# Kernel tuning notes

Measured on AMD Instinct MI355X. Metric: run time of the kernel, lower is better.

The kernel has to match this reference:

```python
import jax, jax.numpy as jnp
import numpy as np
import math

B, N, CS, CZ = 1, 512, 384, 128
GD = 16            # ipa_conf.c_hidden -> num 3D groups G
CH = GD * 3        # per-head hidden = 48
H = 8
PQ, PV = 8, 12
NF = 4             # num_frequencies
INF, EPS = 1e5, 1e-8
CZ4 = CZ // 4


def base_frequencies(num_freqs=NF, base=8.0, max_freq=1.0):
    fs = [min(base ** (-2 * i / num_freqs) * max_freq, max_freq) for i in range(num_freqs)]
    return jnp.asarray(fs, dtype=jnp.float32)


def hat(v):
    # v: [..., 3] -> skew-symmetric [..., 3, 3]
    x, y, z = v[..., 0], v[..., 1], v[..., 2]
    o = jnp.zeros_like(x)
    return jnp.stack([
        jnp.stack([o, -z, y], -1),
        jnp.stack([z, o, -x], -1),
        jnp.stack([-y, x, o], -1)], -2)


def setup_inputs() -> dict:
    key = jax.random.key(0)
    ks = jax.random.split(key, 24)
    std = 0.02
    hc = CH * H
    hpkv = H * (PQ + PV) * 3
    inp = {
        's': jax.random.normal(ks[0], (B, N, CS), jnp.float32),
        'z': jax.random.normal(ks[1], (B, N, N, CZ), jnp.float32),
        'rotvec': jax.random.normal(ks[2], (B, N, 3), jnp.float32),
        'mask': jnp.ones((B, N), jnp.float32),
        'wq': jax.random.normal(ks[3], (CS, hc), jnp.float32) * std,
        'bq': jnp.zeros((hc,), jnp.float32),
        'wkv': jax.random.normal(ks[4], (CS, 2 * hc), jnp.float32) * std,
        'bkv': jnp.zeros((2 * hc,), jnp.float32),
        'wkvp': jax.random.normal(ks[5], (CS, hpkv), jnp.float32) * std,
        'bkvp': jnp.zeros((hpkv,), jnp.float32),
        'wb': jax.random.normal(ks[6], (CZ, H), jnp.float32) * std,
        'bb': jnp.zeros((H,), jnp.float32),
        'wdz': jax.random.normal(ks[7], (CZ, CZ4), jnp.float32) * std,
        'bdz': jnp.zeros((CZ4,), jnp.float32),
        'wout': jax.random.normal(ks[8], (H * (CZ4 + CH + PV * 4), CS), jnp.float32) * std,
        'bout': jnp.zeros((CS,), jnp.float32),
        'log_freq_adj': jax.random.normal(ks[9], (NF,), jnp.float32) * std,
        'group_weights': jax.random.normal(ks[10], (GD,), jnp.float32) * std,
        'freq_weights': jnp.full((NF,), 1.0 / NF, jnp.float32),
    }
    return inp


def reference(s, z, rotvec, mask, wq, bq, wkv, bkv, wkvp, bkvp, wb, bb,
              wdz, bdz, wout, bout, log_freq_adj, group_weights, freq_weights):
    G = GD
    # projections
    q = (s @ wq + bq).reshape(B, N, H, CH)
    kv = (s @ wkv + bkv).reshape(B, N, H, 2 * CH)
    k, v = kv[..., :CH], kv[..., CH:]
    P = PQ + PV
    kvp = (s @ wkvp + bkvp).reshape(B, N, 3, H * P)      # torch split(...,3)+stack(-1)
    kvp = jnp.moveaxis(kvp, -2, -1).reshape(B, N, H, P, 3)
    v_pts = kvp[..., PQ:, :]                             # [B,N,H,PV,3]
    bias = z @ wb + bb                                   # [B,N,N,H]
    # RoPE-inspired multi-frequency Rodrigues rotations
    nrm = jnp.linalg.norm(rotvec, axis=-1, keepdims=True)
    angle = nrm + 1e-8                                   # [B,N,1]
    axis = rotvec / jnp.maximum(nrm, 1e-12)
    freqs = base_frequencies() * jnp.exp(log_freq_adj)   # [F]
    theta = angle * freqs                                # [B,N,F]
    K = hat(axis)                                        # [B,N,3,3]
    K2 = K @ K
    sin_t = jnp.sin(theta)[..., None, None]              # [B,N,F,1,1]
    cos_t = jnp.cos(theta)[..., None, None]
    I3 = jnp.eye(3, dtype=s.dtype)
    R = I3 + sin_t * K[:, :, None] + (1.0 - cos_t) * K2[:, :, None]  # [B,N,F,3,3]
    qg = q.reshape(B, N, H, G, 3)
    kg = k.reshape(B, N, H, G, 3)
    q_rot = jnp.einsum('bnfij,bnhgj->bnhgfi', R, qg)     # [B,N,H,G,F,3]
    k_rot = jnp.einsum('bnfij,bnhgj->bnhgfi', R, kg)
    # aggregation weights (sum over groups, softmax-weighted freqs)
    freq_w = jax.nn.softmax(freq_weights)
    group_w = jax.nn.softplus(group_weights) * math.sqrt(1.0 / G)
    qw = q_rot * freq_w[None, None, None, None, :, None] * group_w[None, None, None, :, None, None]
    scores = jnp.einsum('bihgfc,bjhgfc->bhij', qw, k_rot) / math.sqrt(3.0)
    a = scores + math.sqrt(1.0 / 3.0) * jnp.transpose(bias, (0, 3, 1, 2))
    sq_mask = INF * (mask[:, :, None] * mask[:, None, :] - 1.0)
    a = jax.nn.softmax(a + sq_mask[:, None], axis=-1)    # [B,H,N,N]
    # outputs
    o = jnp.einsum('bhij,bjhc->bihc', a, v).reshape(B, N, H * CH)
    o_pt = jnp.einsum('bhij,bjhpc->bihpc', a, v_pts)     # [B,N,H,PV,3]
    o_pt_norm = jnp.sqrt(jnp.sum(o_pt ** 2, -1) + EPS).reshape(B, N, H * PV)
    o_pt_flat = o_pt.reshape(B, N, H * PV, 3)
    pair_z = z @ wdz + bdz                               # [B,N,N,CZ4]
    o_pair = jnp.einsum('bhij,bijc->bihc', a, pair_z).reshape(B, N, H * CZ4)
    feats = jnp.concatenate([o, o_pt_flat[..., 0], o_pt_flat[..., 1],
                             o_pt_flat[..., 2], o_pt_norm, o_pair], axis=-1)
    return feats @ wout + bout                           # [B,N,CS]
```

## Files before the change

kernel.cpp:

```cpp
#include <hip/hip_runtime.h>
#include <math.h>


#define OFF_PROJ 0
#define SZ_PROJ (512*1632)
#define OFF_QW (OFF_PROJ + SZ_PROJ)
#define SZ_QW (8*512*192)
#define OFF_KST (OFF_QW + SZ_QW)
#define OFF_V (OFF_KST + SZ_QW)
#define SZ_V (512*384)
#define OFF_VP (OFF_V + SZ_V)
#define SZ_VP (512*288)
#define OFF_A (OFF_VP + SZ_VP)
#define SZ_A (8*512*512)
#define OFF_FEATS (OFF_A + SZ_A)
#define SZ_FEATS (512*1024)
#define OFF_PART (OFF_FEATS + SZ_FEATS)
#define SZ_PART (8*512*384)

__global__ __launch_bounds__(256) void proj_kernel(
    const float* __restrict__ s, const float* __restrict__ wq, const float* __restrict__ bq,
    const float* __restrict__ wkv, const float* __restrict__ bkv,
    const float* __restrict__ wkvp, const float* __restrict__ bkvp,
    float* __restrict__ proj)
{
  __shared__ float sT[384][34];
  int ct = blockIdx.x;
  int i0 = blockIdx.y * 32;
  int col0 = ct * 64;
  const float* W; const float* bias; int wld, wcol0;
  if (col0 < 384)       { W = wq;   bias = bq;   wld = 384; wcol0 = col0; }
  else if (col0 < 1152) { W = wkv;  bias = bkv;  wld = 768; wcol0 = col0 - 384; }
  else                  { W = wkvp; bias = bkvp; wld = 480; wcol0 = col0 - 1152; }
  int t = threadIdx.x;
  #pragma unroll
  for (int r = 0; r < 12; r++){
    int e = t + 256*r;
    int i = e & 31;
    int k4 = e >> 5;
    float4 v = *(const float4*)(s + (size_t)(i0 + i)*384 + k4*4);
    sT[k4*4+0][i] = v.x; sT[k4*4+1][i] = v.y; sT[k4*4+2][i] = v.z; sT[k4*4+3][i] = v.w;
  }
  __syncthreads();
  int cr = t & 15;
  int ipair = t >> 4;
  int ii = ipair * 2;
  int wc = wcol0 + cr*4;
  bool valid = (wc + 4 <= wld);
  int wcc = valid ? wc : (wld - 4);
  float acc[2][4];
  #pragma unroll
  for (int q = 0; q < 2; q++)
    #pragma unroll
    for (int p = 0; p < 4; p++) acc[q][p] = 0.f;
  #pragma unroll 4
  for (int k = 0; k < 384; k++){
    float2 a2 = *(const float2*)&sT[k][ii];
    float4 w4 = *(const float4*)(W + (size_t)k*wld + wcc);
    acc[0][0] = fmaf(a2.x, w4.x, acc[0][0]);
    acc[0][1] = fmaf(a2.x, w4.y, acc[0][1]);
    acc[0][2] = fmaf(a2.x, w4.z, acc[0][2]);
    acc[0][3] = fmaf(a2.x, w4.w, acc[0][3]);
    acc[1][0] = fmaf(a2.y, w4.x, acc[1][0]);
    acc[1][1] = fmaf(a2.y, w4.y, acc[1][1]);
    acc[1][2] = fmaf(a2.y, w4.z, acc[1][2]);
    acc[1][3] = fmaf(a2.y, w4.w, acc[1][3]);
  }
  if (valid){
    float4 bv = *(const float4*)(bias + wc);
    #pragma unroll
    for (int q = 0; q < 2; q++){
      int row = i0 + ii + q;
      float4 o;
      o.x = acc[q][0] + bv.x; o.y = acc[q][1] + bv.y;
      o.z = acc[q][2] + bv.z; o.w = acc[q][3] + bv.w;
      *(float4*)(proj + (size_t)row*1632 + col0 + cr*4) = o;
    }
  }
}

__global__ __launch_bounds__(128) void node_kernel(
    const float* __restrict__ proj, const float* __restrict__ rotvec,
    const float* __restrict__ lfa, const float* __restrict__ gwts, const float* __restrict__ fwts,
    float* __restrict__ Qw, float* __restrict__ Kst, float* __restrict__ V, float* __restrict__ VP)
{
  int i = blockIdx.x, t = threadIdx.x;
  const float* pr = proj + (size_t)i*1632;
  float rx = rotvec[i*3], ry = rotvec[i*3+1], rz = rotvec[i*3+2];
  float nrm = sqrtf(rx*rx + ry*ry + rz*rz);
  float angle = nrm + 1e-8f;
  float inv = 1.0f / fmaxf(nrm, 1e-12f);
  float ax = rx*inv, ay = ry*inv, az = rz*inv;
  float f0 = fwts[0], f1 = fwts[1], f2 = fwts[2], f3 = fwts[3];
  float mfw = fmaxf(fmaxf(f0,f1), fmaxf(f2,f3));
  float e0 = expf(f0-mfw), e1 = expf(f1-mfw), e2 = expf(f2-mfw), e3 = expf(f3-mfw);
  float esum = e0+e1+e2+e3;
  float fw[4] = {e0/esum, e1/esum, e2/esum, e3/esum};
  float fq[4] = { 1.0f*expf(lfa[0]), 0.35355339059327373f*expf(lfa[1]),
                  0.125f*expf(lfa[2]), 0.04419417382415922f*expf(lfa[3]) };
  int h = t >> 4, g = t & 15;
  float gw = log1pf(expf(gwts[g])) * 0.25f;
  float q0 = pr[h*48 + g*3 + 0], q1 = pr[h*48 + g*3 + 1], q2 = pr[h*48 + g*3 + 2];
  float k0 = pr[384 + h*96 + g*3 + 0], k1 = pr[384 + h*96 + g*3 + 1], k2 = pr[384 + h*96 + g*3 + 2];
  #pragma unroll
  for (int f = 0; f < 4; f++){
    float th = angle * fq[f];
    float sn = sinf(th), cs = cosf(th), omc = 1.0f - cs;
    float r00 = cs + omc*ax*ax,       r01 = omc*ax*ay - sn*az,  r02 = omc*ax*az + sn*ay;
    float r10 = omc*ay*ax + sn*az,    r11 = cs + omc*ay*ay,     r12 = omc*ay*az - sn*ax;
    float r20 = omc*az*ax - sn*ay,    r21 = omc*az*ay + sn*ax,  r22 = cs + omc*az*az;
    float qr0 = r00*q0 + r01*q1 + r02*q2;
    float qr1 = r10*q0 + r11*q1 + r12*q2;
    float qr2 = r20*q0 + r21*q1 + r22*q2;
    float kr0 = r00*k0 + r01*k1 + r02*k2;
    float kr1 = r10*k0 + r11*k1 + r12*k2;
    float kr2 = r20*k0 + r21*k1 + r22*k2;
    float sc = fw[f] * gw * 0.57735026918962576f;
    int base = (h*512 + i)*192 + (g*4 + f)*3;
    Qw[base+0] = qr0*sc; Qw[base+1] = qr1*sc; Qw[base+2] = qr2*sc;
    Kst[base+0] = kr0;   Kst[base+1] = kr1;   Kst[base+2] = kr2;
  }
  for (int c = t; c < 384; c += 128){
    int hh = c / 48, cc = c % 48;
    V[(size_t)i*384 + c] = pr[384 + hh*96 + 48 + cc];
  }
  for (int qx = t; qx < 288; qx += 128){
    int ch = qx / 3, c3 = qx % 3;
    int hh = ch / 12, p = ch % 12;
    VP[(size_t)i*288 + qx] = pr[1152 + c3*160 + hh*20 + 8 + p];
  }
}

__global__ __launch_bounds__(256) void zbias_kernel(
    const float* __restrict__ z, const float* __restrict__ wb, const float* __restrict__ bb,
    float* __restrict__ biasS)
{
  __shared__ float zs[8*1032];
  __shared__ float Wl[8*132];
  int i = blockIdx.y;
  int jt = blockIdx.x;
  int t = threadIdx.x;
  for (int r = 0; r < 4; r++){
    int e = t + 256*r;
    int ch = e & 7, k = e >> 3;
    Wl[ch*132 + k] = wb[k*8 + ch];
  }
  int cg = t >> 6, jg = t & 63;
  int ch0 = cg*2;
  float acc[2][4];
  #pragma unroll
  for (int c = 0; c < 2; c++)
    #pragma unroll
    for (int q = 0; q < 4; q++) acc[c][q] = 0.f;
  const float* zrow = z + ((size_t)i*512 + jt*256)*128;
  for (int kt = 0; kt < 4; kt++){
    __syncthreads();
    #pragma unroll
    for (int r = 0; r < 8; r++){
      int j = (t & 63) + 64*(r & 3);
      int kq = (t >> 6) + 4*(r >> 2);
      float4 v = *(const float4*)(zrow + (size_t)j*128 + kt*32 + kq*4);
      *(float4*)&zs[kq*1032 + j*4] = v;
    }
    __syncthreads();
    const float* wl0 = Wl + ch0*132 + kt*32;
    const float* wl1 = wl0 + 132;
    #pragma unroll
    for (int kq = 0; kq < 8; kq++){
      float4 w0 = *(const float4*)(wl0 + kq*4);
      float4 w1 = *(const float4*)(wl1 + kq*4);
      #pragma unroll
      for (int q = 0; q < 4; q++){
        float4 zv = *(const float4*)&zs[kq*1032 + (q*64 + jg)*4];
        acc[0][q] = fmaf(zv.x, w0.x, acc[0][q]);
        acc[0][q] = fmaf(zv.y, w0.y, acc[0][q]);
        acc[0][q] = fmaf(zv.z, w0.z, acc[0][q]);
        acc[0][q] = fmaf(zv.w, w0.w, acc[0][q]);
        acc[1][q] = fmaf(zv.x, w1.x, acc[1][q]);
        acc[1][q] = fmaf(zv.y, w1.y, acc[1][q]);
        acc[1][q] = fmaf(zv.z, w1.z, acc[1][q]);
        acc[1][q] = fmaf(zv.w, w1.w, acc[1][q]);
      }
    }
  }
  float b0 = bb[ch0], b1 = bb[ch0+1];
  #pragma unroll
  for (int q = 0; q < 4; q++){
    int j = jt*256 + q*64 + jg;
    biasS[(size_t)ch0*262144 + i*512 + j]     = 0.57735026918962576f * (acc[0][q] + b0);
    biasS[(size_t)(ch0+1)*262144 + i*512 + j] = 0.57735026918962576f * (acc[1][q] + b1);
  }
}

__global__ __launch_bounds__(256) void scores_kernel(
    const float* __restrict__ Qw, const float* __restrict__ Kst,
    const float* __restrict__ mask, float* A)
{
  __shared__ float Ks[4*2056];
  __shared__ float Qs[4*72];
  int i0 = blockIdx.x * 16;
  int h = blockIdx.y;
  int t = threadIdx.x;
  int ig = t >> 6, jl = t & 63;
  const float* Kb = Kst + (size_t)h*512*192;
  const float* Qb = Qw + (size_t)(h*512 + i0)*192;
  float acc[4][8];
  #pragma unroll
  for (int q = 0; q < 4; q++)
    #pragma unroll
    for (int jt = 0; jt < 8; jt++) acc[q][jt] = 0.f;
  for (int kc = 0; kc < 12; kc++){
    __syncthreads();
    {
      int k4 = t >> 6;
      #pragma unroll
      for (int r = 0; r < 8; r++){
        int j = (t & 63) + 64*r;
        float4 v = *(const float4*)(Kb + (size_t)j*192 + kc*16 + k4*4);
        *(float4*)&Ks[k4*2056 + j*4] = v;
      }
    }
    if (t < 64){
      int qi = t >> 2, k4 = t & 3;
      float4 v = *(const float4*)(Qb + (size_t)qi*192 + kc*16 + k4*4);
      *(float4*)&Qs[k4*72 + qi*4] = v;
    }
    __syncthreads();
    #pragma unroll
    for (int k4 = 0; k4 < 4; k4++){
      float4 qf[4];
      #pragma unroll
      for (int q = 0; q < 4; q++)
        qf[q] = *(const float4*)&Qs[k4*72 + (ig*4+q)*4];
      #pragma unroll
      for (int jt = 0; jt < 8; jt++){
        float4 kf = *(const float4*)&Ks[k4*2056 + (jt*64 + jl)*4];
        #pragma unroll
        for (int q = 0; q < 4; q++){
          acc[q][jt] = fmaf(qf[q].x, kf.x, acc[q][jt]);
          acc[q][jt] = fmaf(qf[q].y, kf.y, acc[q][jt]);
          acc[q][jt] = fmaf(qf[q].z, kf.z, acc[q][jt]);
          acc[q][jt] = fmaf(qf[q].w, kf.w, acc[q][jt]);
        }
      }
    }
  }
  int j0 = jl;
  float mj[8];
  #pragma unroll
  for (int jt = 0; jt < 8; jt++) mj[jt] = mask[jt*64 + j0];
  #pragma unroll
  for (int q = 0; q < 4; q++){
    int i = i0 + ig*4 + q;
    float mi = mask[i];
    #pragma unroll
    for (int jt = 0; jt < 8; jt++){
      float b = A[((size_t)h*512 + i)*512 + jt*64 + j0];
      acc[q][jt] += b + 100000.0f*(mi*mj[jt] - 1.0f);
    }
    float m = acc[q][0];
    #pragma unroll
    for (int jt = 1; jt < 8; jt++) m = fmaxf(m, acc[q][jt]);
    for (int off = 32; off > 0; off >>= 1) m = fmaxf(m, __shfl_xor(m, off));
    float ssum = 0.f;
    #pragma unroll
    for (int jt = 0; jt < 8; jt++){ acc[q][jt] = expf(acc[q][jt] - m); ssum += acc[q][jt]; }
    for (int off = 32; off > 0; off >>= 1) ssum += __shfl_xor(ssum, off);
    float invs = 1.0f / ssum;
    #pragma unroll
    for (int jt = 0; jt < 8; jt++){
      A[((size_t)h*512 + i)*512 + jt*64 + j0] = acc[q][jt] * invs;
    }
  }
}

__global__ __launch_bounds__(256) void paircomb_kernel(
    const float* __restrict__ A, const float* __restrict__ z,
    const float* __restrict__ wdz, const float* __restrict__ bdz,
    float* __restrict__ feats)
{
  __shared__ float a_s[2*512*10];
  __shared__ float Y_s[2*8*132];
  int i0 = blockIdx.x * 2;
  int t = threadIdx.x;
  for (int r = 0; r < 32; r++){
    int e = t + 256*r;
    int hh = e >> 10, il = (e >> 9) & 1, j = e & 511;
    a_s[(il*512 + j)*10 + hh] = A[((size_t)hh*512 + i0 + il)*512 + j];
  }
  __syncthreads();
  int il = t >> 7, u = t & 127, hg = u >> 5, k4 = u & 31;
  const float* zb = z + ((size_t)(i0 + il)*512)*128 + k4*4;
  const float* asb = a_s + il*5120 + hg*2;
  float acc0[4], acc1[4];
  #pragma unroll
  for (int m = 0; m < 4; m++){ acc0[m] = 0.f; acc1[m] = 0.f; }
  #pragma unroll 8
  for (int j = 0; j < 512; j++){
    float2 a2 = *(const float2*)&asb[j*10];
    float4 zv = *(const float4*)(zb + (size_t)j*128);
    acc0[0] = fmaf(a2.x, zv.x, acc0[0]);
    acc0[1] = fmaf(a2.x, zv.y, acc0[1]);
    acc0[2] = fmaf(a2.x, zv.z, acc0[2]);
    acc0[3] = fmaf(a2.x, zv.w, acc0[3]);
    acc1[0] = fmaf(a2.y, zv.x, acc1[0]);
    acc1[1] = fmaf(a2.y, zv.y, acc1[1]);
    acc1[2] = fmaf(a2.y, zv.z, acc1[2]);
    acc1[3] = fmaf(a2.y, zv.w, acc1[3]);
  }
  float4 y0, y1;
  y0.x = acc0[0]; y0.y = acc0[1]; y0.z = acc0[2]; y0.w = acc0[3];
  y1.x = acc1[0]; y1.y = acc1[1]; y1.z = acc1[2]; y1.w = acc1[3];
  *(float4*)&Y_s[((il*8) + hg*2 + 0)*132 + k4*4] = y0;
  *(float4*)&Y_s[((il*8) + hg*2 + 1)*132 + k4*4] = y1;
  __syncthreads();
  {
    int il2 = t >> 7, u2 = t & 127, hh = u2 >> 4, cp = u2 & 15;
    const float* Yr = Y_s + (il2*8 + hh)*132;
    float s0 = bdz[cp*2], s1 = bdz[cp*2+1];
    #pragma unroll 8
    for (int k = 0; k < 128; k++){
      float yv = Yr[k];
      float2 w2 = *(const float2*)(wdz + (size_t)k*32 + cp*2);
      s0 = fmaf(yv, w2.x, s0);
      s1 = fmaf(yv, w2.y, s1);
    }
    float* fp = feats + (size_t)(i0 + il2)*1024 + 768 + hh*32 + cp*2;
    fp[0] = s0; fp[1] = s1;
  }
}

__global__ __launch_bounds__(256) void ovcomb_kernel(
    const float* __restrict__ A, const float* __restrict__ V, const float* __restrict__ VP,
    float* __restrict__ feats)
{
  __shared__ float a_s2[8*64*2];
  __shared__ float opt_s[2][292];
  int i0 = blockIdx.x * 2;
  int t = threadIdx.x;
  bool act = (t < 168);
  const float* base = V; int stride = 384; int hh = 0;
  if (act){
    int ch = t*4;
    if (ch < 384){ hh = ch/48; base = V + ch; stride = 384; }
    else { int qq = ch - 384; hh = qq/36; base = VP + qq; stride = 288; }
  }
  float acc0[4], acc1[4];
  #pragma unroll
  for (int m = 0; m < 4; m++){ acc0[m] = 0.f; acc1[m] = 0.f; }
  for (int jt = 0; jt < 8; jt++){
    __syncthreads();
    #pragma unroll
    for (int r = 0; r < 4; r++){
      int e = t + 256*r;
      int eh = e >> 7, il = (e >> 6) & 1, jj = e & 63;
      a_s2[(eh*64 + jj)*2 + il] = A[((size_t)eh*512 + i0 + il)*512 + jt*64 + jj];
    }
    __syncthreads();
    if (act){
      const float* bj = base + (size_t)(jt*64)*stride;
      #pragma unroll 4
      for (int jj = 0; jj < 64; jj++){
        float2 a2 = *(const float2*)&a_s2[(hh*64 + jj)*2];
        float4 v4 = *(const float4*)(bj + (size_t)jj*stride);
        acc0[0] = fmaf(a2.x, v4.x, acc0[0]);
        acc0[1] = fmaf(a2.x, v4.y, acc0[1]);
        acc0[2] = fmaf(a2.x, v4.z, acc0[2]);
        acc0[3] = fmaf(a2.x, v4.w, acc0[3]);
        acc1[0] = fmaf(a2.y, v4.x, acc1[0]);
        acc1[1] = fmaf(a2.y, v4.y, acc1[1]);
        acc1[2] = fmaf(a2.y, v4.z, acc1[2]);
        acc1[3] = fmaf(a2.y, v4.w, acc1[3]);
      }
    }
  }
  if (act){
    int ch = t*4;
    if (ch < 384){
      float4 o0, o1;
      o0.x = acc0[0]; o0.y = acc0[1]; o0.z = acc0[2]; o0.w = acc0[3];
      o1.x = acc1[0]; o1.y = acc1[1]; o1.z = acc1[2]; o1.w = acc1[3];
      *(float4*)&feats[(size_t)i0*1024 + ch] = o0;
      *(float4*)&feats[(size_t)(i0+1)*1024 + ch] = o1;
    } else {
      int qq = ch - 384;
      #pragma unroll
      for (int m = 0; m < 4; m++){
        opt_s[0][qq + m] = acc0[m];
        opt_s[1][qq + m] = acc1[m];
      }
    }
  }
  __syncthreads();
  if (t < 192){
    int il = t / 96, p = t % 96;
    float x = opt_s[il][p*3], y = opt_s[il][p*3+1], zz = opt_s[il][p*3+2];
    float* fr = feats + (size_t)(i0 + il)*1024;
    fr[384 + p] = x;
    fr[480 + p] = y;
    fr[576 + p] = zz;
    fr[672 + p] = sqrtf(x*x + y*y + zz*zz + 1e-8f);
  }
}

__global__ __launch_bounds__(256) void outgemm_kernel(
    const float* __restrict__ feats, const float* __restrict__ wout,
    float* __restrict__ part)
{
  __shared__ float fA[32*68];
  __shared__ float fB[32*68];
  int ct = blockIdx.x;
  int it = blockIdx.y;
  int sk = blockIdx.z;
  int i0 = it*64, c0 = ct*64, k0 = sk*128;
  int t = threadIdx.x;
  int ir = t >> 4, cr = t & 15;
  float acc[4][4];
  #pragma unroll
  for (int q = 0; q < 4; q++)
    #pragma unroll
    for (int p = 0; p < 4; p++) acc[q][p] = 0.f;
  for (int kt = 0; kt < 128; kt += 32){
    __syncthreads();
    #pragma unroll
    for (int r = 0; r < 2; r++){
      int e = t + 256*r;
      int i = e & 63, kq = e >> 6;
      float4 v = *(const float4*)(feats + (size_t)(i0 + i)*1024 + k0 + kt + kq*4);
      fA[(kq*4+0)*68 + i] = v.x; fA[(kq*4+1)*68 + i] = v.y;
      fA[(kq*4+2)*68 + i] = v.z; fA[(kq*4+3)*68 + i] = v.w;
    }
    #pragma unroll
    for (int r = 0; r < 2; r++){
      int e = t + 256*r;
      int kk = e >> 4, c4 = e & 15;
      float4 v = *(const float4*)(wout + (size_t)(k0 + kt + kk)*384 + c0 + c4*4);
      *(float4*)&fB[kk*68 + c4*4] = v;
    }
    __syncthreads();
    #pragma unroll 8
    for (int k = 0; k < 32; k++){
      float4 a4 = *(const float4*)&fA[k*68 + ir*4];
      float4 b4 = *(const float4*)&fB[k*68 + cr*4];
      acc[0][0] = fmaf(a4.x, b4.x, acc[0][0]);
      acc[0][1] = fmaf(a4.x, b4.y, acc[0][1]);
      acc[0][2] = fmaf(a4.x, b4.z, acc[0][2]);
      acc[0][3] = fmaf(a4.x, b4.w, acc[0][3]);
      acc[1][0] = fmaf(a4.y, b4.x, acc[1][0]);
      acc[1][1] = fmaf(a4.y, b4.y, acc[1][1]);
      acc[1][2] = fmaf(a4.y, b4.z, acc[1][2]);
      acc[1][3] = fmaf(a4.y, b4.w, acc[1][3]);
      acc[2][0] = fmaf(a4.z, b4.x, acc[2][0]);
      acc[2][1] = fmaf(a4.z, b4.y, acc[2][1]);
      acc[2][2] = fmaf(a4.z, b4.z, acc[2][2]);
      acc[2][3] = fmaf(a4.z, b4.w, acc[2][3]);
      acc[3][0] = fmaf(a4.w, b4.x, acc[3][0]);
      acc[3][1] = fmaf(a4.w, b4.y, acc[3][1]);
      acc[3][2] = fmaf(a4.w, b4.z, acc[3][2]);
      acc[3][3] = fmaf(a4.w, b4.w, acc[3][3]);
    }
  }
  float* pb = part + ((size_t)sk*512 + i0)*384 + c0;
  #pragma unroll
  for (int q = 0; q < 4; q++){
    float4 o;
    o.x = acc[q][0]; o.y = acc[q][1]; o.z = acc[q][2]; o.w = acc[q][3];
    *(float4*)&pb[(size_t)(ir*4 + q)*384 + cr*4] = o;
  }
}

__global__ __launch_bounds__(256) void outreduce_kernel(
    const float* __restrict__ part, const float* __restrict__ bout,
    float* __restrict__ out)
{
  int e = blockIdx.x*256 + threadIdx.x;
  float4 acc = *(const float4*)(bout + (e % 96)*4);
  #pragma unroll
  for (int sk = 0; sk < 8; sk++){
    float4 p = *(const float4*)(part + (size_t)sk*196608 + (size_t)e*4);
    acc.x += p.x; acc.y += p.y; acc.z += p.z; acc.w += p.w;
  }
  *(float4*)(out + (size_t)e*4) = acc;
}

extern "C" void kernel_launch(void* const* d_in, const int* in_sizes, int n_in,
                              void* d_out, int out_size, void* d_ws, size_t ws_size,
                              hipStream_t stream)
{
  const float* s    = (const float*)d_in[0];
  const float* z    = (const float*)d_in[1];
  const float* rotv = (const float*)d_in[2];
  const float* mask = (const float*)d_in[3];
  const float* wq   = (const float*)d_in[4];
  const float* bq   = (const float*)d_in[5];
  const float* wkv  = (const float*)d_in[6];
  const float* bkv  = (const float*)d_in[7];
  const float* wkvp = (const float*)d_in[8];
  const float* bkvp = (const float*)d_in[9];
  const float* wb   = (const float*)d_in[10];
  const float* bb   = (const float*)d_in[11];
  const float* wdz  = (const float*)d_in[12];
  const float* bdz  = (const float*)d_in[13];
  const float* wout = (const float*)d_in[14];
  const float* bout = (const float*)d_in[15];
  const float* lfa  = (const float*)d_in[16];
  const float* gwts = (const float*)d_in[17];
  const float* fwts = (const float*)d_in[18];
  float* out = (float*)d_out;
  float* ws  = (float*)d_ws;

  float* proj  = ws + OFF_PROJ;
  float* Qw    = ws + OFF_QW;
  float* Kst   = ws + OFF_KST;
  float* V     = ws + OFF_V;
  float* VP    = ws + OFF_VP;
  float* A     = ws + OFF_A;
  float* feats = ws + OFF_FEATS;
  float* part  = ws + OFF_PART;

  proj_kernel     <<<dim3(26, 16), 256, 0, stream>>>(s, wq, bq, wkv, bkv, wkvp, bkvp, proj);
  node_kernel     <<<dim3(512),    128, 0, stream>>>(proj, rotv, lfa, gwts, fwts, Qw, Kst, V, VP);
  zbias_kernel    <<<dim3(2, 512), 256, 0, stream>>>(z, wb, bb, A);
  scores_kernel   <<<dim3(32, 8),  256, 0, stream>>>(Qw, Kst, mask, A);
  paircomb_kernel <<<dim3(256),    256, 0, stream>>>(A, z, wdz, bdz, feats);
  ovcomb_kernel   <<<dim3(256),    256, 0, stream>>>(A, V, VP, feats);
  outgemm_kernel  <<<dim3(6, 8, 8),256, 0, stream>>>(feats, wout, part);
  outreduce_kernel<<<dim3(192),    256, 0, stream>>>(part, bout, out);
}
```

Before: 422.3 us.

## Fuse pair and value attention-output kernels; halve scores tile rows per block

Merges the pair-z combination and value/point combination kernels into one attnout kernel. The fused kernel reuses the attention rows already staged in shared memory, so A is read once instead of twice and one launch goes away. The scores kernel now handles 8 query rows per block instead of 16, doubling its grid to 512 blocks for better CU occupancy. It also loads the z-bias and mask into the accumulators before the dot-product loop. In exchange, the K tile is loaded twice as often in total, and the fused kernel runs more serial work per block.

After: 423.6 us. No clear change (+0.3%).

```diff
diff --git a/kernel.cpp b/kernel.cpp
--- a/kernel.cpp
+++ b/kernel.cpp
@@ -197,18 +197,26 @@
     const float* __restrict__ mask, float* A)
 {
   __shared__ float Ks[4*2056];
-  __shared__ float Qs[4*72];
-  int i0 = blockIdx.x * 16;
+  __shared__ float Qs[4*40];
+  int i0 = blockIdx.x * 8;
   int h = blockIdx.y;
   int t = threadIdx.x;
   int ig = t >> 6, jl = t & 63;
   const float* Kb = Kst + (size_t)h*512*192;
   const float* Qb = Qw + (size_t)(h*512 + i0)*192;
-  float acc[4][8];
-  #pragma unroll
-  for (int q = 0; q < 4; q++)
-    #pragma unroll
-    for (int jt = 0; jt < 8; jt++) acc[q][jt] = 0.f;
+  float acc[2][8];
+  float mj[8];
+  #pragma unroll
+  for (int jt = 0; jt < 8; jt++) mj[jt] = mask[jt*64 + jl];
+  #pragma unroll
+  for (int q = 0; q < 2; q++){
+    int i = i0 + ig*2 + q;
+    float mi = mask[i];
+    #pragma unroll
+    for (int jt = 0; jt < 8; jt++){
+      acc[q][jt] = A[((size_t)h*512 + i)*512 + jt*64 + jl] + 100000.0f*(mi*mj[jt] - 1.0f);
+    }
+  }
   for (int kc = 0; kc < 12; kc++){
     __syncthreads();
     {
@@ -220,23 +228,23 @@
         *(float4*)&Ks[k4*2056 + j*4] = v;
       }
     }
-    if (t < 64){
+    if (t < 32){
       int qi = t >> 2, k4 = t & 3;
       float4 v = *(const float4*)(Qb + (size_t)qi*192 + kc*16 + k4*4);
-      *(float4*)&Qs[k4*72 + qi*4] = v;
+      *(float4*)&Qs[k4*40 + qi*4] = v;
     }
     __syncthreads();
     #pragma unroll
     for (int k4 = 0; k4 < 4; k4++){
-      float4 qf[4];
+      float4 qf[2];
       #pragma unroll
-      for (int q = 0; q < 4; q++)
-        qf[q] = *(const float4*)&Qs[k4*72 + (ig*4+q)*4];
+      for (int q = 0; q < 2; q++)
+        qf[q] = *(const float4*)&Qs[k4*40 + (ig*2+q)*4];
       #pragma unroll
       for (int jt = 0; jt < 8; jt++){
         float4 kf = *(const float4*)&Ks[k4*2056 + (jt*64 + jl)*4];
         #pragma unroll
-        for (int q = 0; q < 4; q++){
+        for (int q = 0; q < 2; q++){
           acc[q][jt] = fmaf(qf[q].x, kf.x, acc[q][jt]);
           acc[q][jt] = fmaf(qf[q].y, kf.y, acc[q][jt]);
           acc[q][jt] = fmaf(qf[q].z, kf.z, acc[q][jt]);
@@ -245,19 +253,9 @@
       }
     }
   }
-  int j0 = jl;
-  float mj[8];
-  #pragma unroll
-  for (int jt = 0; jt < 8; jt++) mj[jt] = mask[jt*64 + j0];
-  #pragma unroll
-  for (int q = 0; q < 4; q++){
-    int i = i0 + ig*4 + q;
-    float mi = mask[i];
-    #pragma unroll
-    for (int jt = 0; jt < 8; jt++){
-      float b = A[((size_t)h*512 + i)*512 + jt*64 + j0];
-      acc[q][jt] += b + 100000.0f*(mi*mj[jt] - 1.0f);
-    }
+  #pragma unroll
+  for (int q = 0; q < 2; q++){
+    int i = i0 + ig*2 + q;
     float m = acc[q][0];
     #pragma unroll
     for (int jt = 1; jt < 8; jt++) m = fmaxf(m, acc[q][jt]);
@@ -269,18 +267,20 @@
     float invs = 1.0f / ssum;
     #pragma unroll
     for (int jt = 0; jt < 8; jt++){
-      A[((size_t)h*512 + i)*512 + jt*64 + j0] = acc[q][jt] * invs;
-    }
-  }
-}
-
-__global__ __launch_bounds__(256) void paircomb_kernel(
+      A[((size_t)h*512 + i)*512 + jt*64 + jl] = acc[q][jt] * invs;
+    }
+  }
+}
+
+__global__ __launch_bounds__(256) void attnout_kernel(
     const float* __restrict__ A, const float* __restrict__ z,
     const float* __restrict__ wdz, const float* __restrict__ bdz,
+    const float* __restrict__ V, const float* __restrict__ VP,
     float* __restrict__ feats)
 {
   __shared__ float a_s[2*512*10];
   __shared__ float Y_s[2*8*132];
+  __shared__ float opt_s[2][292];
   int i0 = blockIdx.x * 2;
   int t = threadIdx.x;
   for (int r = 0; r < 32; r++){
@@ -289,34 +289,33 @@
     a_s[(il*512 + j)*10 + hh] = A[((size_t)hh*512 + i0 + il)*512 + j];
   }
   __syncthreads();
-  int il = t >> 7, u = t & 127, hg = u >> 5, k4 = u & 31;
-  const float* zb = z + ((size_t)(i0 + il)*512)*128 + k4*4;
-  const float* asb = a_s + il*5120 + hg*2;
-  float acc0[4], acc1[4];
-  #pragma unroll
-  for (int m = 0; m < 4; m++){ acc0[m] = 0.f; acc1[m] = 0.f; }
-  #pragma unroll 8
-  for (int j = 0; j < 512; j++){
-    float2 a2 = *(const float2*)&asb[j*10];
-    float4 zv = *(const float4*)(zb + (size_t)j*128);
-    acc0[0] = fmaf(a2.x, zv.x, acc0[0]);
-    acc0[1] = fmaf(a2.x, zv.y, acc0[1]);
-    acc0[2] = fmaf(a2.x, zv.z, acc0[2]);
-    acc0[3] = fmaf(a2.x, zv.w, acc0[3]);
-    acc1[0] = fmaf(a2.y, zv.x, acc1[0]);
-    acc1[1] = fmaf(a2.y, zv.y, acc1[1]);
-    acc1[2] = fmaf(a2.y, zv.z, acc1[2]);
-    acc1[3] = fmaf(a2.y, zv.w, acc1[3]);
-  }
-  float4 y0, y1;
-  y0.x = acc0[0]; y0.y = acc0[1]; y0.z = acc0[2]; y0.w = acc0[3];
-  y1.x = acc1[0]; y1.y = acc1[1]; y1.z = acc1[2]; y1.w = acc1[3];
-  *(float4*)&Y_s[((il*8) + hg*2 + 0)*132 + k4*4] = y0;
-  *(float4*)&Y_s[((il*8) + hg*2 + 1)*132 + k4*4] = y1;
+  {
+    int il = t >> 7, u = t & 127, hg = u >> 5, k4 = u & 31;
+    const float* zb = z + ((size_t)(i0 + il)*512)*128 + k4*4;
+    const float* asb = a_s + il*5120 + hg*2;
+    float acc0[4], acc1[4];
+    #pragma unroll
+    for (int m = 0; m < 4; m++){ acc0[m] = 0.f; acc1[m] = 0.f; }
+    #pragma unroll 8
+    for (int j = 0; j < 512; j++){
+      float2 a2 = *(const float2*)&asb[j*10];
+      float4 zv = *(const float4*)(zb + (size_t)j*128);
+      acc0[0] = fmaf(a2.x, zv.x, acc0[0]);
+      acc0[1] = fmaf(a2.x, zv.y, acc0[1]);
+      acc0[2] = fmaf(a2.x, zv.z, acc0[2]);
+      acc0[3] = fmaf(a2.x, zv.w, acc0[3]);
+      acc1[0] = fmaf(a2.y, zv.x, acc1[0]);
+      acc1[1] = fmaf(a2.y, zv.y, acc1[1]);
+      acc1[2] = fmaf(a2.y, zv.z, acc1[2]);
+      acc1[3] = fmaf(a2.y, zv.w, acc1[3]);
+    }
+    *(float4*)&Y_s[((il*8) + hg*2 + 0)*132 + k4*4] = make_float4(acc0[0],acc0[1],acc0[2],acc0[3]);
+    *(float4*)&Y_s[((il*8) + hg*2 + 1)*132 + k4*4] = make_float4(acc1[0],acc1[1],acc1[2],acc1[3]);
+  }
   __syncthreads();
   {
-    int il2 = t >> 7, u2 = t & 127, hh = u2 >> 4, cp = u2 & 15;
-    const float* Yr = Y_s + (il2*8 + hh)*132;
+    int il = t >> 7, u = t & 127, hh = u >> 4, cp = u & 15;
+    const float* Yr = Y_s + (il*8 + hh)*132;
     float s0 = bdz[cp*2], s1 = bdz[cp*2+1];
     #pragma unroll 8
     for (int k = 0; k < 128; k++){
@@ -325,69 +324,47 @@
       s0 = fmaf(yv, w2.x, s0);
       s1 = fmaf(yv, w2.y, s1);
     }
-    float* fp = feats + (size_t)(i0 + il2)*1024 + 768 + hh*32 + cp*2;
+    float* fp = feats + (size_t)(i0 + il)*1024 + 768 + hh*32 + cp*2;
     fp[0] = s0; fp[1] = s1;
   }
-}
-
-__global__ __launch_bounds__(256) void ovcomb_kernel(
-    const float* __restrict__ A, const float* __restrict__ V, const float* __restrict__ VP,
-    float* __restrict__ feats)
-{
-  __shared__ float a_s2[8*64*2];
-  __shared__ float opt_s[2][292];
-  int i0 = blockIdx.x * 2;
-  int t = threadIdx.x;
-  bool act = (t < 168);
-  const float* base = V; int stride = 384; int hh = 0;
-  if (act){
+  {
+    bool act = (t < 168);
+    const float* base = V; int stride = 384; int hh = 0;
     int ch = t*4;
-    if (ch < 384){ hh = ch/48; base = V + ch; stride = 384; }
-    else { int qq = ch - 384; hh = qq/36; base = VP + qq; stride = 288; }
-  }
-  float acc0[4], acc1[4];
-  #pragma unroll
-  for (int m = 0; m < 4; m++){ acc0[m] = 0.f; acc1[m] = 0.f; }
-  for (int jt = 0; jt < 8; jt++){
-    __syncthreads();
-    #pragma unroll
-    for (int r = 0; r < 4; r++){
-      int e = t + 256*r;
-      int eh = e >> 7, il = (e >> 6) & 1, jj = e & 63;
-      a_s2[(eh*64 + jj)*2 + il] = A[((size_t)eh*512 + i0 + il)*512 + jt*64 + jj];
-    }
-    __syncthreads();
     if (act){
-      const float* bj = base + (size_t)(jt*64)*stride;
+      if (ch < 384){ hh = ch/48; base = V + ch; stride = 384; }
+      else { int qq = ch - 384; hh = qq/36; base = VP + qq; stride = 288; }
+    }
+    float acc0[4], acc1[4];
+    #pragma unroll
+    for (int m = 0; m < 4; m++){ acc0[m] = 0.f; acc1[m] = 0.f; }
+    if (act){
+      const float* a0 = a_s + hh;
+      const float* a1 = a_s + 5120 + hh;
       #pragma unroll 4
-      for (int jj = 0; jj < 64; jj++){
-        float2 a2 = *(const float2*)&a_s2[(hh*64 + jj)*2];
-        float4 v4 = *(const float4*)(bj + (size_t)jj*stride);
-        acc0[0] = fmaf(a2.x, v4.x, acc0[0]);
-        acc0[1] = fmaf(a2.x, v4.y, acc0[1]);
-        acc0[2] = fmaf(a2.x, v4.z, acc0[2]);
-        acc0[3] = fmaf(a2.x, v4.w, acc0[3]);
-        acc1[0] = fmaf(a2.y, v4.x, acc1[0]);
-        acc1[1] = fmaf(a2.y, v4.y, acc1[1]);
-        acc1[2] = fmaf(a2.y, v4.z, acc1[2]);
-        acc1[3] = fmaf(a2.y, v4.w, acc1[3]);
+      for (int j = 0; j < 512; j++){
+        float ax = a0[j*10];
+        float ay = a1[j*10];
+        float4 v4 = *(const float4*)(base + (size_t)j*stride);
+        acc0[0] = fmaf(ax, v4.x, acc0[0]);
+        acc0[1] = fmaf(ax, v4.y, acc0[1]);
+        acc0[2] = fmaf(ax, v4.z, acc0[2]);
+        acc0[3] = fmaf(ax, v4.w, acc0[3]);
+        acc1[0] = fmaf(ay, v4.x, acc1[0]);
+        acc1[1] = fmaf(ay, v4.y, acc1[1]);
+        acc1[2] = fmaf(ay, v4.z, acc1[2]);
+        acc1[3] = fmaf(ay, v4.w, acc1[3]);
       }
-    }
-  }
-  if (act){
-    int ch = t*4;
-    if (ch < 384){
-      float4 o0, o1;
-      o0.x = acc0[0]; o0.y = acc0[1]; o0.z = acc0[2]; o0.w = acc0[3];
-      o1.x = acc1[0]; o1.y = acc1[1]; o1.z = acc1[2]; o1.w = acc1[3];
-      *(float4*)&feats[(size_t)i0*1024 + ch] = o0;
-      *(float4*)&feats[(size_t)(i0+1)*1024 + ch] = o1;
-    } else {
-      int qq = ch - 384;
-      #pragma unroll
-      for (int m = 0; m < 4; m++){
-        opt_s[0][qq + m] = acc0[m];
-        opt_s[1][qq + m] = acc1[m];
+      if (ch < 384){
+        *(float4*)&feats[(size_t)i0*1024 + ch]     = make_float4(acc0[0],acc0[1],acc0[2],acc0[3]);
+        *(float4*)&feats[(size_t)(i0+1)*1024 + ch] = make_float4(acc1[0],acc1[1],acc1[2],acc1[3]);
+      } else {
+        int qq = ch - 384;
+        #pragma unroll
+        for (int m = 0; m < 4; m++){
+          opt_s[0][qq + m] = acc0[m];
+          opt_s[1][qq + m] = acc1[m];
+        }
       }
     }
   }
@@ -521,9 +498,8 @@
   proj_kernel     <<<dim3(26, 16), 256, 0, stream>>>(s, wq, bq, wkv, bkv, wkvp, bkvp, proj);
   node_kernel     <<<dim3(512),    128, 0, stream>>>(proj, rotv, lfa, gwts, fwts, Qw, Kst, V, VP);
   zbias_kernel    <<<dim3(2, 512), 256, 0, stream>>>(z, wb, bb, A);
-  scores_kernel   <<<dim3(32, 8),  256, 0, stream>>>(Qw, Kst, mask, A);
-  paircomb_kernel <<<dim3(256),    256, 0, stream>>>(A, z, wdz, bdz, feats);
-  ovcomb_kernel   <<<dim3(256),    256, 0, stream>>>(A, V, VP, feats);
+  scores_kernel   <<<dim3(64, 8),  256, 0, stream>>>(Qw, Kst, mask, A);
+  attnout_kernel  <<<dim3(256),    256, 0, stream>>>(A, z, wdz, bdz, V, VP, feats);
   outgemm_kernel  <<<dim3(6, 8, 8),256, 0, stream>>>(feats, wout, part);
   outreduce_kernel<<<dim3(192),    256, 0, stream>>>(part, bout, out);
 }
```
